# Performance work log

Measured on AMD Instinct MI355X. Metric: run time of the kernel, lower is better.

## Reference

```python
import jax, jax.numpy as jnp
import numpy as np

N_NODES = 100000
N_EDGES = 3200000
K_STEPS = 10
ALPHA = 0.1


def setup_inputs() -> dict:
    key = jax.random.key(0)
    k1, k2, k3, k4 = jax.random.split(key, 4)
    x = jax.random.normal(k1, (N_NODES, 512), dtype=jnp.float32)
    edge_index = jax.random.randint(k2, (2, N_EDGES), 0, N_NODES, dtype=jnp.int32)
    # Glorot-ish scaled params for lin1/lin2
    W1 = jax.random.normal(k3, (512, 256), dtype=jnp.float32) * (1.0 / np.sqrt(512))
    b1 = jnp.zeros((256,), dtype=jnp.float32)
    W2 = jax.random.normal(k4, (256, 64), dtype=jnp.float32) * (1.0 / np.sqrt(256))
    b2 = jnp.zeros((64,), dtype=jnp.float32)
    return {"x": x, "edge_index": edge_index, "W1": W1, "b1": b1, "W2": W2, "b2": b2}


def _gcn_norm(edge_index, num_nodes):
    # Add self-loops, compute symmetric normalization coefficients (PyG gcn_norm).
    loop = jnp.arange(num_nodes, dtype=edge_index.dtype)
    row = jnp.concatenate([edge_index[0], loop])
    col = jnp.concatenate([edge_index[1], loop])
    deg = jax.ops.segment_sum(jnp.ones_like(col, dtype=jnp.float32), col,
                              num_segments=num_nodes)
    dinv = jnp.where(deg > 0, jax.lax.rsqrt(deg), 0.0)
    norm = dinv[row] * dinv[col]  # [E + N]
    return row, col, norm


def reference(x, edge_index, W1, b1, W2, b2):
    # Inference mode: dropout is identity (training=False).
    h = jax.nn.relu(x @ W1 + b1) @ W2 + b2  # [N, out]
    num_nodes = x.shape[0]
    row, col, norm = _gcn_norm(edge_index, num_nodes)

    def step(z, _):
        msg = norm[:, None] * z[row]  # gather + scale, [E+N, out]
        agg = jax.ops.segment_sum(msg, col, num_segments=num_nodes)
        return (1.0 - ALPHA) * agg + ALPHA * h, None

    z, _ = jax.lax.scan(step, h, None, length=K_STEPS)
    return jax.nn.log_softmax(z, axis=1)
```

## Files before the change

kernel.cpp:

```cpp
#include <hip/hip_runtime.h>
#include <hip/hip_bf16.h>

typedef __attribute__((ext_vector_type(8))) short   short8;
typedef __attribute__((ext_vector_type(4))) short   shortx4;
typedef __attribute__((ext_vector_type(8))) __bf16  bf16x8;
typedef __attribute__((ext_vector_type(4))) float   floatx4;

__device__ inline float bf2f(short u) {
    return __builtin_bit_cast(float, (unsigned)((unsigned short)u) << 16);
}
__device__ inline short f2bf(float f) {
    return __builtin_bit_cast(short, __float2bfloat16(f));
}

__device__ inline void gll16(const void* g, void* l) {
    __builtin_amdgcn_global_load_lds(
        (const __attribute__((address_space(1))) unsigned int*)g,
        (__attribute__((address_space(3))) unsigned int*)l, 16, 0, 0);
}


__global__ void count_kernel(const int* __restrict__ col, int* __restrict__ icnt, int E) {
    int e = blockIdx.x * 256 + threadIdx.x;
    if (e < E) atomicAdd(&icnt[col[e]], 1);
}

__global__ void dinv_cursor_kernel(const int* __restrict__ icnt, float* __restrict__ dinv,
                                   int* __restrict__ cursor, int N) {
    int i = blockIdx.x * 256 + threadIdx.x;
    if (i < N) { dinv[i] = rsqrtf((float)(icnt[i] + 1)); cursor[i] = 0; }
}


__global__ __launch_bounds__(256) void blocksum_kernel(const int* __restrict__ icnt,
                                                       int* __restrict__ bsum, int N) {
    int b = blockIdx.x, t = threadIdx.x;
    int base = b * 1024 + t * 4;
    int s = 0;
    if (base + 3 < N) {
        int4 v = *(const int4*)&icnt[base];
        s = v.x + v.y + v.z + v.w;
    } else {
        for (int i = 0; i < 4; i++) if (base + i < N) s += icnt[base + i];
    }
    __shared__ int red[256];
    red[t] = s;
    __syncthreads();
    for (int o = 128; o > 0; o >>= 1) {
        if (t < o) red[t] += red[t + o];
        __syncthreads();
    }
    if (t == 0) bsum[b] = red[0];
}

__global__ __launch_bounds__(128) void bscan_kernel(int* __restrict__ bsum,
                                                    int* __restrict__ offs, int NB, int N) {
    __shared__ int sh[128];
    int t = threadIdx.x;
    int v = (t < NB) ? bsum[t] : 0;
    sh[t] = v;
    __syncthreads();
    for (int o = 1; o < 128; o <<= 1) {
        int u = (t >= o) ? sh[t - o] : 0;
        __syncthreads();
        sh[t] += u;
        __syncthreads();
    }
    if (t < NB) bsum[t] = sh[t] - v;
    if (t == 127) offs[N] = sh[127];
}

__global__ __launch_bounds__(256) void offs_kernel(const int* __restrict__ icnt,
                                                   const int* __restrict__ bsum,
                                                   int* __restrict__ offs, int N) {
    int b = blockIdx.x, t = threadIdx.x;
    int base = b * 1024 + t * 4;
    int v[4]; int s = 0;
#pragma unroll
    for (int i = 0; i < 4; i++) {
        int idx = base + i;
        v[i] = (idx < N) ? icnt[idx] : 0;
        s += v[i];
    }
    __shared__ int sh[256];
    sh[t] = s;
    __syncthreads();
    for (int o = 1; o < 256; o <<= 1) {
        int u = (t >= o) ? sh[t - o] : 0;
        __syncthreads();
        sh[t] += u;
        __syncthreads();
    }
    int off = bsum[b] + sh[t] - s;
#pragma unroll
    for (int i = 0; i < 4; i++) {
        int idx = base + i;
        if (idx < N) { offs[idx] = off; off += v[i]; }
    }
}

__global__ void scatter_kernel(const int* __restrict__ row, const int* __restrict__ col,
                               const int* __restrict__ offs, int* __restrict__ cursor,
                               int* __restrict__ csr, int E) {
    int e = blockIdx.x * 256 + threadIdx.x;
    if (e < E) {
        int c = col[e];
        int p = offs[c] + atomicAdd(&cursor[c], 1);
        csr[p] = row[e];
    }
}


__global__ void w1_tile_kernel(const float* __restrict__ src,
                               __hip_bfloat16* __restrict__ dst) {
    int t = blockIdx.x * 256 + threadIdx.x;
    if (t < 512 * 256) {
        int k = t >> 8, n = t & 255;
        int kc = k >> 5, kl = k & 31;
        int slot = kl >> 3, pos = kl & 7;
        int sl = slot ^ ((n >> 1) & 3);
        dst[kc * 8192 + n * 32 + sl * 8 + pos] = __float2bfloat16(src[t]);
    }
}

__global__ void transpose_cvt_kernel(const float* __restrict__ src,
                                     __hip_bfloat16* __restrict__ dst, int K, int N) {
    int t = blockIdx.x * 256 + threadIdx.x;
    if (t < K * N) { int k = t / N, n = t % N; dst[n * K + k] = __float2bfloat16(src[t]); }
}


__global__ __launch_bounds__(256) void mlp_kernel(
    const float* __restrict__ x, const __hip_bfloat16* __restrict__ W1Tt,
    const float* __restrict__ b1, const __hip_bfloat16* __restrict__ W2T,
    const float* __restrict__ b2, __hip_bfloat16* __restrict__ h, int M)
{
    __shared__ __align__(16) short lds[16384];
    short* Ts = lds;

    const int t = threadIdx.x;
    const int lane = t & 63, wave = t >> 6;
    const int lm = lane & 15, quad = lane >> 4;
    const int block_m = blockIdx.x * 64;
    const short* w2s = (const short*)W2T;
    const char*  w1b = (const char*)W1Tt;

    const int grow = block_m + wave * 16 + lm;
    const bool rok = grow < M;
    const float* xrow = x + (size_t)grow * 512 + quad * 8;
    const floatx4 z4 = (floatx4){0.f, 0.f, 0.f, 0.f};

    const int chunk_base = wave * 4;
    const int gl_off = lane * 16;

    auto stageB = [&](int kc, int buf) {
#pragma unroll
        for (int it = 0; it < 4; it++) {
            int chunk = chunk_base + it;
            gll16(w1b + (size_t)kc * 16384 + chunk * 1024 + gl_off,
                  &lds[buf * 8192 + chunk * 512]);
        }
    };

    floatx4 accA[16];
#pragma unroll
    for (int i = 0; i < 16; i++) accA[i] = z4;

    stageB(0, 0);
    floatx4 a0  = rok ? *(const floatx4*)xrow       : z4;
    floatx4 a1  = rok ? *(const floatx4*)(xrow + 4) : z4;
    floatx4 na0 = z4, na1 = z4;

    const int boff = lm * 32 + ((quad ^ ((lm >> 1) & 3)) << 3);

    __syncthreads();

    for (int kc = 0; kc < 16; kc++) {
        if (kc < 15) {
            stageB(kc + 1, (kc + 1) & 1);
            const float* p = xrow + (kc + 1) * 32;
            na0 = rok ? *(const floatx4*)p       : z4;
            na1 = rok ? *(const floatx4*)(p + 4) : z4;
        }
        short8 afs;
#pragma unroll
        for (int j = 0; j < 4; j++) { afs[j] = f2bf(a0[j]); afs[4 + j] = f2bf(a1[j]); }
        bf16x8 af = __builtin_bit_cast(bf16x8, afs);
        const short* bb = &lds[(kc & 1) * 8192];
#pragma unroll
        for (int nt = 0; nt < 16; nt++) {
            bf16x8 bfr = __builtin_bit_cast(bf16x8, *(const short8*)&bb[nt * 512 + boff]);
            accA[nt] = __builtin_amdgcn_mfma_f32_16x16x32_bf16(af, bfr, accA[nt], 0, 0, 0);
        }
        a0 = na0; a1 = na1;
        __syncthreads();
    }

    floatx4 accB[4];
#pragma unroll
    for (int j = 0; j < 4; j++) accB[j] = z4;

#pragma unroll
    for (int s = 0; s < 4; s++) {
        __syncthreads();
#pragma unroll
        for (int ntl = 0; ntl < 4; ntl++) {
            int nt = s * 4 + ntl;
            float bv = b1[nt * 16 + lm];
#pragma unroll
            for (int r = 0; r < 4; r++) {
                int rowl = wave * 16 + quad * 4 + r;
                Ts[rowl * 72 + ntl * 16 + lm] = f2bf(fmaxf(accA[nt][r] + bv, 0.f));
            }
        }
        __syncthreads();
#pragma unroll
        for (int kk = 0; kk < 2; kk++) {
            bf16x8 af2 = __builtin_bit_cast(bf16x8,
                *(const short8*)&Ts[(wave * 16 + lm) * 72 + kk * 32 + quad * 8]);
#pragma unroll
            for (int nt = 0; nt < 4; nt++) {
                bf16x8 bfr = __builtin_bit_cast(bf16x8,
                    *(const short8*)&w2s[(size_t)(nt * 16 + lm) * 256 + s * 64 + kk * 32 + quad * 8]);
                accB[nt] = __builtin_amdgcn_mfma_f32_16x16x32_bf16(af2, bfr, accB[nt], 0, 0, 0);
            }
        }
    }

#pragma unroll
    for (int nt = 0; nt < 4; nt++) {
        int colg = nt * 16 + lm;
        float bv = b2[colg];
#pragma unroll
        for (int r = 0; r < 4; r++) {
            int rowg = block_m + wave * 16 + quad * 4 + r;
            if (rowg < M)
                h[(size_t)rowg * 64 + colg] = __float2bfloat16(accB[nt][r] + bv);
        }
    }
}


__global__ __launch_bounds__(256) void prop_kernel(
    const __hip_bfloat16* __restrict__ z_in, const __hip_bfloat16* __restrict__ h,
    const float* __restrict__ dinv, const int* __restrict__ offs,
    const int* __restrict__ csr, __hip_bfloat16* __restrict__ z_out,
    float* __restrict__ out, int N, int last)
{
    int node = blockIdx.x * 4 + (threadIdx.x >> 6);
    if (node >= N) return;
    int lane = threadIdx.x & 63;
    int g = lane >> 3, i = lane & 7;
    const short* zs = (const short*)z_in;
    const short* hs = (const short*)h;
    float di = dinv[node];
    int s = offs[node], e = offs[node + 1];
    float acc[8] = {0.f, 0.f, 0.f, 0.f, 0.f, 0.f, 0.f, 0.f};

    for (int j0 = s; j0 < e; j0 += 64) {
        int jj = j0 + lane;
        int nbr = 0; float dn = 0.f;
        if (jj < e) { nbr = csr[jj]; dn = dinv[nbr]; }
        int cnt = min(64, e - j0);
        bool more = cnt > 32;

        int nb[8]; float wv[8];
#pragma unroll
        for (int tt = 0; tt < 8; tt++) {
            int src = tt * 8 + g;
            nb[tt] = __shfl(nbr, src);
            wv[tt] = __shfl(dn, src);
        }

        short8 zv[8];
#pragma unroll
        for (int tt = 0; tt < 4; tt++)
            zv[tt] = *(const short8*)&zs[(size_t)nb[tt] * 64 + i * 8];
        if (more) {
#pragma unroll
            for (int tt = 4; tt < 8; tt++)
                zv[tt] = *(const short8*)&zs[(size_t)nb[tt] * 64 + i * 8];
        }
#pragma unroll
        for (int tt = 0; tt < 4; tt++)
#pragma unroll
            for (int j = 0; j < 8; j++)
                acc[j] = fmaf(wv[tt], bf2f(zv[tt][j]), acc[j]);
        if (more) {
#pragma unroll
            for (int tt = 4; tt < 8; tt++)
#pragma unroll
                for (int j = 0; j < 8; j++)
                    acc[j] = fmaf(wv[tt], bf2f(zv[tt][j]), acc[j]);
        }
    }
#pragma unroll
    for (int j = 0; j < 8; j++) {
        acc[j] += __shfl_xor(acc[j], 8);
        acc[j] += __shfl_xor(acc[j], 16);
        acc[j] += __shfl_xor(acc[j], 32);
    }

    short8 zv = *(const short8*)&zs[(size_t)node * 64 + i * 8];
    short8 hv = *(const short8*)&hs[(size_t)node * 64 + i * 8];
    float v[8];
#pragma unroll
    for (int j = 0; j < 8; j++)
        v[j] = 0.9f * (di * acc[j] + di * di * bf2f(zv[j])) + 0.1f * bf2f(hv[j]);

    if (!last) {
        if (g == 0) {
            short8 o8;
#pragma unroll
            for (int j = 0; j < 8; j++) o8[j] = f2bf(v[j]);
            *(short8*)&((short*)z_out)[(size_t)node * 64 + i * 8] = o8;
        }
    } else {
        float m = v[0];
#pragma unroll
        for (int j = 1; j < 8; j++) m = fmaxf(m, v[j]);
        m = fmaxf(m, __shfl_xor(m, 1));
        m = fmaxf(m, __shfl_xor(m, 2));
        m = fmaxf(m, __shfl_xor(m, 4));
        float ss = 0.f;
#pragma unroll
        for (int j = 0; j < 8; j++) ss += expf(v[j] - m);
        ss += __shfl_xor(ss, 1);
        ss += __shfl_xor(ss, 2);
        ss += __shfl_xor(ss, 4);
        float ls = m + logf(ss);
        if (g == 0) {
            floatx4 o0, o1;
#pragma unroll
            for (int j = 0; j < 4; j++) { o0[j] = v[j] - ls; o1[j] = v[4 + j] - ls; }
            *(floatx4*)&out[(size_t)node * 64 + i * 8]     = o0;
            *(floatx4*)&out[(size_t)node * 64 + i * 8 + 4] = o1;
        }
    }
}


extern "C" void kernel_launch(void* const* d_in, const int* in_sizes, int n_in,
                              void* d_out, int out_size, void* d_ws, size_t ws_size,
                              hipStream_t stream) {
    const float* x  = (const float*)d_in[0];
    const int*   ei = (const int*)d_in[1];
    const float* W1 = (const float*)d_in[2];
    const float* b1 = (const float*)d_in[3];
    const float* W2 = (const float*)d_in[4];
    const float* b2 = (const float*)d_in[5];
    float* out = (float*)d_out;

    const int FIN = 512, FH = 256, FO = 64;
    const int N = in_sizes[0] / FIN;
    const int E = in_sizes[1] / 2;
    const int* erow = ei;
    const int* ecol = ei + E;

    char* w = (char*)d_ws;
    size_t o = 0;
    auto take = [&](size_t bytes) -> void* {
        void* p = w + o;
        o += (bytes + 511) & ~(size_t)511;
        return p;
    };
    int*   icnt   = (int*)  take((size_t)N * 4);
    float* dinv   = (float*)take((size_t)N * 4);
    int*   offs   = (int*)  take((size_t)(N + 1) * 4);
    int*   cursor = (int*)  take((size_t)N * 4);
    int*   csr    = (int*)  take((size_t)E * 4);
    int*   bsum   = (int*)  take((size_t)128 * 4);
    __hip_bfloat16* W1Tt = (__hip_bfloat16*)take((size_t)FIN * FH * 2);
    __hip_bfloat16* W2T  = (__hip_bfloat16*)take((size_t)FH * FO * 2);
    __hip_bfloat16* hbuf = (__hip_bfloat16*)take((size_t)N * FO * 2);
    __hip_bfloat16* zA   = (__hip_bfloat16*)take((size_t)N * FO * 2);
    __hip_bfloat16* zB   = (__hip_bfloat16*)out;

    const int NB = (N + 1023) / 1024;

    (void)hipMemsetAsync(icnt, 0, (size_t)N * 4, stream);
    count_kernel<<<(E + 255) / 256, 256, 0, stream>>>(ecol, icnt, E);
    dinv_cursor_kernel<<<(N + 255) / 256, 256, 0, stream>>>(icnt, dinv, cursor, N);
    blocksum_kernel<<<NB, 256, 0, stream>>>(icnt, bsum, N);
    bscan_kernel<<<1, 128, 0, stream>>>(bsum, offs, NB, N);
    offs_kernel<<<NB, 256, 0, stream>>>(icnt, bsum, offs, N);
    scatter_kernel<<<(E + 255) / 256, 256, 0, stream>>>(erow, ecol, offs, cursor, csr, E);
    w1_tile_kernel<<<(FIN * FH + 255) / 256, 256, 0, stream>>>(W1, W1Tt);
    transpose_cvt_kernel<<<(FH * FO + 255) / 256, 256, 0, stream>>>(W2, W2T, FH, FO);

    mlp_kernel<<<(N + 63) / 64, 256, 0, stream>>>(x, W1Tt, b1, W2T, b2, hbuf, N);

    const __hip_bfloat16* zin = hbuf;
    for (int k = 0; k < 10; k++) {
        int last = (k == 9);
        __hip_bfloat16* zout = (k & 1) ? zB : zA;
        prop_kernel<<<(N + 3) / 4, 256, 0, stream>>>(zin, hbuf, dinv, offs, csr,
                                                     zout, out, N, last);
        zin = zout;
    }
}
```

Measured before the change: 1.244 ms.

## Split node features into four 16-column planes so each propagation pass gathers an L2-resident slice

The MLP output and the propagation buffers now use a plane-major layout of four 16-feature slices, each holding every node. A new propagation kernel assigns each block to one slice, so the randomly gathered working set per pass is a quarter of the full feature matrix and has a better chance of staying in cache. Each wave now handles 32 neighbours per load with 32-byte gathers, and interleaved block indexing keeps neighbouring blocks on different slices. The last step reads all four planes so log-softmax can be applied per row. In exchange the CSR offsets and indices are read four times per step, and the smaller gathers may use less memory bandwidth per request.

```diff
diff --git a/kernel.cpp b/kernel.cpp
--- a/kernel.cpp
+++ b/kernel.cpp
@@ -229,30 +229,95 @@
 
 #pragma unroll
     for (int nt = 0; nt < 4; nt++) {
-        int colg = nt * 16 + lm;
-        float bv = b2[colg];
+        float bv = b2[nt * 16 + lm];
 #pragma unroll
         for (int r = 0; r < 4; r++) {
             int rowg = block_m + wave * 16 + quad * 4 + r;
             if (rowg < M)
-                h[(size_t)rowg * 64 + colg] = __float2bfloat16(accB[nt][r] + bv);
-        }
-    }
-}
-
-
-__global__ __launch_bounds__(256) void prop_kernel(
-    const __hip_bfloat16* __restrict__ z_in, const __hip_bfloat16* __restrict__ h,
+                h[((size_t)nt * M + rowg) * 16 + lm] = __float2bfloat16(accB[nt][r] + bv);
+        }
+    }
+}
+
+
+__global__ __launch_bounds__(256) void prop_fast_kernel(
+    const short* __restrict__ zq_in, const short* __restrict__ hq,
     const float* __restrict__ dinv, const int* __restrict__ offs,
-    const int* __restrict__ csr, __hip_bfloat16* __restrict__ z_out,
-    float* __restrict__ out, int N, int last)
+    const int* __restrict__ csr, short* __restrict__ zq_out, int N)
+{
+    const int bid = blockIdx.x;
+    const int q = (bid >> 1) & 3;
+    const int nbk = (bid >> 3) * 2 + (bid & 1);
+    const int node = nbk * 4 + (threadIdx.x >> 6);
+    if (node >= N) return;
+    const int lane = threadIdx.x & 63;
+    const int grp = lane >> 1, i2 = lane & 1;
+    const short* zp = zq_in + (size_t)q * N * 16;
+    const short* hp = hq    + (size_t)q * N * 16;
+    float di = dinv[node];
+    int s = offs[node], e = offs[node + 1];
+    float acc[8] = {0.f, 0.f, 0.f, 0.f, 0.f, 0.f, 0.f, 0.f};
+
+    for (int j0 = s; j0 < e; j0 += 64) {
+        int jj = j0 + lane;
+        int nbr = 0; float dn = 0.f;
+        if (jj < e) { nbr = csr[jj]; dn = dinv[nbr]; }
+        bool more = (e - j0) > 32;
+
+        int   nb0 = __shfl(nbr, grp);
+        float w0  = __shfl(dn,  grp);
+        int   nb1 = __shfl(nbr, 32 + grp);
+        float w1  = __shfl(dn,  32 + grp);
+
+        short8 zv0 = *(const short8*)&zp[(size_t)nb0 * 16 + i2 * 8];
+        if (more) {
+            short8 zv1 = *(const short8*)&zp[(size_t)nb1 * 16 + i2 * 8];
+#pragma unroll
+            for (int j = 0; j < 8; j++) {
+                acc[j] = fmaf(w0, bf2f(zv0[j]), acc[j]);
+                acc[j] = fmaf(w1, bf2f(zv1[j]), acc[j]);
+            }
+        } else {
+#pragma unroll
+            for (int j = 0; j < 8; j++)
+                acc[j] = fmaf(w0, bf2f(zv0[j]), acc[j]);
+        }
+    }
+#pragma unroll
+    for (int j = 0; j < 8; j++) {
+        acc[j] += __shfl_xor(acc[j], 2);
+        acc[j] += __shfl_xor(acc[j], 4);
+        acc[j] += __shfl_xor(acc[j], 8);
+        acc[j] += __shfl_xor(acc[j], 16);
+        acc[j] += __shfl_xor(acc[j], 32);
+    }
+
+    short8 zv = *(const short8*)&zp[(size_t)node * 16 + i2 * 8];
+    short8 hv = *(const short8*)&hp[(size_t)node * 16 + i2 * 8];
+    if (lane < 2) {
+        short8 o8;
+#pragma unroll
+        for (int j = 0; j < 8; j++) {
+            float v = 0.9f * (di * acc[j] + di * di * bf2f(zv[j])) + 0.1f * bf2f(hv[j]);
+            o8[j] = f2bf(v);
+        }
+        *(short8*)&zq_out[((size_t)q * N + node) * 16 + i2 * 8] = o8;
+    }
+}
+
+
+__global__ __launch_bounds__(256) void prop_last_kernel(
+    const short* __restrict__ zq_in, const short* __restrict__ hq,
+    const float* __restrict__ dinv, const int* __restrict__ offs,
+    const int* __restrict__ csr, float* __restrict__ out, int N)
 {
     int node = blockIdx.x * 4 + (threadIdx.x >> 6);
     if (node >= N) return;
     int lane = threadIdx.x & 63;
     int g = lane >> 3, i = lane & 7;
-    const short* zs = (const short*)z_in;
-    const short* hs = (const short*)h;
+    const int pl = i >> 1, ph = i & 1;
+    const short* zp = zq_in + (size_t)pl * N * 16;
+    const short* hp = hq    + (size_t)pl * N * 16;
     float di = dinv[node];
     int s = offs[node], e = offs[node + 1];
     float acc[8] = {0.f, 0.f, 0.f, 0.f, 0.f, 0.f, 0.f, 0.f};
@@ -261,8 +326,7 @@
         int jj = j0 + lane;
         int nbr = 0; float dn = 0.f;
         if (jj < e) { nbr = csr[jj]; dn = dinv[nbr]; }
-        int cnt = min(64, e - j0);
-        bool more = cnt > 32;
+        bool more = (e - j0) > 32;
 
         int nb[8]; float wv[8];
 #pragma unroll
@@ -271,15 +335,14 @@
             nb[tt] = __shfl(nbr, src);
             wv[tt] = __shfl(dn, src);
         }
-
         short8 zv[8];
 #pragma unroll
         for (int tt = 0; tt < 4; tt++)
-            zv[tt] = *(const short8*)&zs[(size_t)nb[tt] * 64 + i * 8];
+            zv[tt] = *(const short8*)&zp[(size_t)nb[tt] * 16 + ph * 8];
         if (more) {
 #pragma unroll
             for (int tt = 4; tt < 8; tt++)
-                zv[tt] = *(const short8*)&zs[(size_t)nb[tt] * 64 + i * 8];
+                zv[tt] = *(const short8*)&zp[(size_t)nb[tt] * 16 + ph * 8];
         }
 #pragma unroll
         for (int tt = 0; tt < 4; tt++)
@@ -301,41 +364,32 @@
         acc[j] += __shfl_xor(acc[j], 32);
     }
 
-    short8 zv = *(const short8*)&zs[(size_t)node * 64 + i * 8];
-    short8 hv = *(const short8*)&hs[(size_t)node * 64 + i * 8];
+    short8 zv = *(const short8*)&zp[(size_t)node * 16 + ph * 8];
+    short8 hv = *(const short8*)&hp[(size_t)node * 16 + ph * 8];
     float v[8];
 #pragma unroll
     for (int j = 0; j < 8; j++)
         v[j] = 0.9f * (di * acc[j] + di * di * bf2f(zv[j])) + 0.1f * bf2f(hv[j]);
 
-    if (!last) {
-        if (g == 0) {
-            short8 o8;
-#pragma unroll
-            for (int j = 0; j < 8; j++) o8[j] = f2bf(v[j]);
-            *(short8*)&((short*)z_out)[(size_t)node * 64 + i * 8] = o8;
-        }
-    } else {
-        float m = v[0];
-#pragma unroll
-        for (int j = 1; j < 8; j++) m = fmaxf(m, v[j]);
-        m = fmaxf(m, __shfl_xor(m, 1));
-        m = fmaxf(m, __shfl_xor(m, 2));
-        m = fmaxf(m, __shfl_xor(m, 4));
-        float ss = 0.f;
-#pragma unroll
-        for (int j = 0; j < 8; j++) ss += expf(v[j] - m);
-        ss += __shfl_xor(ss, 1);
-        ss += __shfl_xor(ss, 2);
-        ss += __shfl_xor(ss, 4);
-        float ls = m + logf(ss);
-        if (g == 0) {
-            floatx4 o0, o1;
-#pragma unroll
-            for (int j = 0; j < 4; j++) { o0[j] = v[j] - ls; o1[j] = v[4 + j] - ls; }
-            *(floatx4*)&out[(size_t)node * 64 + i * 8]     = o0;
-            *(floatx4*)&out[(size_t)node * 64 + i * 8 + 4] = o1;
-        }
+    float m = v[0];
+#pragma unroll
+    for (int j = 1; j < 8; j++) m = fmaxf(m, v[j]);
+    m = fmaxf(m, __shfl_xor(m, 1));
+    m = fmaxf(m, __shfl_xor(m, 2));
+    m = fmaxf(m, __shfl_xor(m, 4));
+    float ss = 0.f;
+#pragma unroll
+    for (int j = 0; j < 8; j++) ss += expf(v[j] - m);
+    ss += __shfl_xor(ss, 1);
+    ss += __shfl_xor(ss, 2);
+    ss += __shfl_xor(ss, 4);
+    float ls = m + logf(ss);
+    if (g == 0) {
+        floatx4 o0, o1;
+#pragma unroll
+        for (int j = 0; j < 4; j++) { o0[j] = v[j] - ls; o1[j] = v[4 + j] - ls; }
+        *(floatx4*)&out[(size_t)node * 64 + i * 8]     = o0;
+        *(floatx4*)&out[(size_t)node * 64 + i * 8 + 4] = o1;
     }
 }
 
@@ -372,9 +426,9 @@
     int*   bsum   = (int*)  take((size_t)128 * 4);
     __hip_bfloat16* W1Tt = (__hip_bfloat16*)take((size_t)FIN * FH * 2);
     __hip_bfloat16* W2T  = (__hip_bfloat16*)take((size_t)FH * FO * 2);
-    __hip_bfloat16* hbuf = (__hip_bfloat16*)take((size_t)N * FO * 2);
-    __hip_bfloat16* zA   = (__hip_bfloat16*)take((size_t)N * FO * 2);
-    __hip_bfloat16* zB   = (__hip_bfloat16*)out;
+    short* hbuf = (short*)take((size_t)N * FO * 2);
+    short* zA   = (short*)take((size_t)N * FO * 2);
+    short* zB   = (short*)out;
 
     const int NB = (N + 1023) / 1024;
 
@@ -388,14 +442,17 @@
     w1_tile_kernel<<<(FIN * FH + 255) / 256, 256, 0, stream>>>(W1, W1Tt);
     transpose_cvt_kernel<<<(FH * FO + 255) / 256, 256, 0, stream>>>(W2, W2T, FH, FO);
 
-    mlp_kernel<<<(N + 63) / 64, 256, 0, stream>>>(x, W1Tt, b1, W2T, b2, hbuf, N);
-
-    const __hip_bfloat16* zin = hbuf;
-    for (int k = 0; k < 10; k++) {
-        int last = (k == 9);
-        __hip_bfloat16* zout = (k & 1) ? zB : zA;
-        prop_kernel<<<(N + 3) / 4, 256, 0, stream>>>(zin, hbuf, dinv, offs, csr,
-                                                     zout, out, N, last);
+    mlp_kernel<<<(N + 63) / 64, 256, 0, stream>>>(x, W1Tt, b1, W2T, b2,
+                                                  (__hip_bfloat16*)hbuf, N);
+
+    const int grid_fast = 8 * ((N + 7) / 8);
+    const short* zin = hbuf;
+    for (int k = 0; k < 9; k++) {
+        short* zout = (k & 1) ? zB : zA;
+        prop_fast_kernel<<<grid_fast, 256, 0, stream>>>(zin, hbuf, dinv, offs, csr,
+                                                        zout, N);
         zin = zout;
     }
-}
+    prop_last_kernel<<<(N + 3) / 4, 256, 0, stream>>>(zin, hbuf, dinv, offs, csr,
+                                                      out, N);
+}
```

New measurement: 2.465 ms. 1.98x slower.
